# Kernel optimization log

Measured on AMD Instinct MI355X. Metric: run time of the kernel, lower is better.

## Reference

```python
import jax, jax.numpy as jnp
import numpy as np

ALPHA = 0.9

def setup_inputs() -> dict:
    key = jax.random.key(0)
    inputs = jax.random.normal(key, (16, 4000, 512), dtype=jnp.float32)
    return {"inputs": inputs}

def reference(inputs) -> jnp.ndarray:
    # y_t = (1-alpha) * y_{t-1} + alpha * x_t, with y_{-1} = 0
    # (matches torch loop: y_0 = alpha * x_0)
    a = jnp.asarray(ALPHA, dtype=inputs.dtype)
    one_minus_a = jnp.asarray(1.0 - ALPHA, dtype=inputs.dtype)
    x_t = jnp.swapaxes(inputs, 0, 1)  # [T, B, C] for scan over time

    def step(carry, x):
        y = one_minus_a * carry + a * x
        return y, y

    init = jnp.zeros(x_t.shape[1:], dtype=inputs.dtype)  # [B, C]
    _, ys = jax.lax.scan(step, init, x_t)  # ys: [T, B, C]
    return jnp.swapaxes(ys, 0, 1)  # [B, T, C]
```

## Files before the change

kernel.cpp:

```cpp
#include <hip/hip_runtime.h>


constexpr int B_ = 16;
constexpr int T_ = 4000;
constexpr int C_ = 512;
constexpr int L_ = 50;
constexpr int W_ = 16;
constexpr int NC4_ = C_ / 4;
constexpr int NCHUNK_ = (T_ + L_ - 1) / L_;

__global__ __launch_bounds__(256) void ema_chunk_scan(const float* __restrict__ x,
                                                      float* __restrict__ y) {
    int g = blockIdx.x * blockDim.x + threadIdx.x;
    int c4 = g & (NC4_ - 1);
    int bt = g >> 7;
    int b  = bt & (B_ - 1);
    int chunk = bt >> 4;
    if (chunk >= NCHUNK_) return;

    int t_write = chunk * L_;
    int t_begin = t_write - W_;
    if (t_begin < 0) t_begin = 0;
    int t_end = t_write + L_;
    if (t_end > T_) t_end = T_;

    const float4* p = (const float4*)(x + ((size_t)b * T_ + t_begin) * C_) + c4;
    float4*       q = (float4*)(y + ((size_t)b * T_ + t_write) * C_) + c4;

    const float a = 0.9f, om = 0.1f;
    float4 acc = make_float4(0.f, 0.f, 0.f, 0.f);

    #pragma unroll 4
    for (int t = t_begin; t < t_write; ++t) {
        float4 xv = *p; p += NC4_;
        acc.x = om * acc.x + a * xv.x;
        acc.y = om * acc.y + a * xv.y;
        acc.z = om * acc.z + a * xv.z;
        acc.w = om * acc.w + a * xv.w;
    }
    #pragma unroll 5
    for (int t = t_write; t < t_end; ++t) {
        float4 xv = *p; p += NC4_;
        acc.x = om * acc.x + a * xv.x;
        acc.y = om * acc.y + a * xv.y;
        acc.z = om * acc.z + a * xv.z;
        acc.w = om * acc.w + a * xv.w;
        *q = acc; q += NC4_;
    }
}

extern "C" void kernel_launch(void* const* d_in, const int* in_sizes, int n_in,
                              void* d_out, int out_size, void* d_ws, size_t ws_size,
                              hipStream_t stream) {
    const float* x = (const float*)d_in[0];
    float* y = (float*)d_out;
    int total_threads = B_ * NC4_ * NCHUNK_;
    int block = 256;
    int grid = (total_threads + block - 1) / block;
    ema_chunk_scan<<<grid, block, 0, stream>>>(x, y);
}
```

Baseline: 253.3 us.

## Batch independent loads per thread and shrink chunks to raise memory-level parallelism

Shortens time chunks from 50 to 20 steps with an 8-step warmup, so many more threads run concurrently. It loads the warmup window and then 10-step batches into register arrays before doing the serial recurrence, so many global loads are in flight at once. Stores are also batched, and launch bounds request higher occupancy. In exchange, the extra warmup reads form a larger fraction of traffic, and register pressure rises. The shorter warmup also truncates history after 8 steps, which relies on the decay factor 0.1.

```diff
diff --git a/kernel.cpp b/kernel.cpp
--- a/kernel.cpp
+++ b/kernel.cpp
@@ -4,48 +4,57 @@
 constexpr int B_ = 16;
 constexpr int T_ = 4000;
 constexpr int C_ = 512;
-constexpr int L_ = 50;
-constexpr int W_ = 16;
+constexpr int L_ = 20;
+constexpr int W_ = 8;
 constexpr int NC4_ = C_ / 4;
-constexpr int NCHUNK_ = (T_ + L_ - 1) / L_;
+constexpr int NCHUNK_ = T_ / L_;
+constexpr int BATCH_ = 10;
 
-__global__ __launch_bounds__(256) void ema_chunk_scan(const float* __restrict__ x,
-                                                      float* __restrict__ y) {
+__global__ __launch_bounds__(256, 8) void ema_chunk_scan(const float* __restrict__ x,
+                                                         float* __restrict__ y) {
     int g = blockIdx.x * blockDim.x + threadIdx.x;
     int c4 = g & (NC4_ - 1);
     int bt = g >> 7;
     int b  = bt & (B_ - 1);
     int chunk = bt >> 4;
-    if (chunk >= NCHUNK_) return;
 
-    int t_write = chunk * L_;
-    int t_begin = t_write - W_;
-    if (t_begin < 0) t_begin = 0;
-    int t_end = t_write + L_;
-    if (t_end > T_) t_end = T_;
-
-    const float4* p = (const float4*)(x + ((size_t)b * T_ + t_begin) * C_) + c4;
-    float4*       q = (float4*)(y + ((size_t)b * T_ + t_write) * C_) + c4;
-
+    int t0 = chunk * L_;
     const float a = 0.9f, om = 0.1f;
     float4 acc = make_float4(0.f, 0.f, 0.f, 0.f);
 
-    #pragma unroll 4
-    for (int t = t_begin; t < t_write; ++t) {
-        float4 xv = *p; p += NC4_;
-        acc.x = om * acc.x + a * xv.x;
-        acc.y = om * acc.y + a * xv.y;
-        acc.z = om * acc.z + a * xv.z;
-        acc.w = om * acc.w + a * xv.w;
+    if (chunk > 0) {
+        const float4* pw = (const float4*)(x + ((size_t)b * T_ + (t0 - W_)) * C_) + c4;
+        float4 wbuf[W_];
+        #pragma unroll
+        for (int i = 0; i < W_; ++i) wbuf[i] = pw[(size_t)i * NC4_];
+        #pragma unroll
+        for (int i = 0; i < W_; ++i) {
+            acc.x = om * acc.x + a * wbuf[i].x;
+            acc.y = om * acc.y + a * wbuf[i].y;
+            acc.z = om * acc.z + a * wbuf[i].z;
+            acc.w = om * acc.w + a * wbuf[i].w;
+        }
     }
-    #pragma unroll 5
-    for (int t = t_write; t < t_end; ++t) {
-        float4 xv = *p; p += NC4_;
-        acc.x = om * acc.x + a * xv.x;
-        acc.y = om * acc.y + a * xv.y;
-        acc.z = om * acc.z + a * xv.z;
-        acc.w = om * acc.w + a * xv.w;
-        *q = acc; q += NC4_;
+
+    const float4* pm = (const float4*)(x + ((size_t)b * T_ + t0) * C_) + c4;
+    float4*       q  = (float4*)(y + ((size_t)b * T_ + t0) * C_) + c4;
+    #pragma unroll
+    for (int blk = 0; blk < L_ / BATCH_; ++blk) {
+        float4 buf[BATCH_];
+        #pragma unroll
+        for (int i = 0; i < BATCH_; ++i) buf[i] = pm[(size_t)i * NC4_];
+        pm += (size_t)BATCH_ * NC4_;
+        #pragma unroll
+        for (int i = 0; i < BATCH_; ++i) {
+            acc.x = om * acc.x + a * buf[i].x;
+            acc.y = om * acc.y + a * buf[i].y;
+            acc.z = om * acc.z + a * buf[i].z;
+            acc.w = om * acc.w + a * buf[i].w;
+            buf[i] = acc;
+        }
+        #pragma unroll
+        for (int i = 0; i < BATCH_; ++i) q[(size_t)i * NC4_] = buf[i];
+        q += (size_t)BATCH_ * NC4_;
     }
 }
 
@@ -56,6 +65,6 @@
     float* y = (float*)d_out;
     int total_threads = B_ * NC4_ * NCHUNK_;
     int block = 256;
-    int grid = (total_threads + block - 1) / block;
+    int grid = total_threads / block;
     ema_chunk_scan<<<grid, block, 0, stream>>>(x, y);
 }
```

New measurement: 236.9 us. 1.07x faster.
